# Optimization experiments

Measured on AMD Instinct MI355X. Metric: run time of the kernel, lower is better.

The kernel has to match this reference:

```python
import jax, jax.numpy as jnp
import numpy as np

B, T, D, H = 32, 4096, 512, 512


def setup_inputs() -> dict:
    key = jax.random.key(0)
    ks = jax.random.split(key, 8)
    s = 1.0 / np.sqrt(D)
    return {
        "hidden_state": jax.random.normal(ks[0], (B, D), jnp.float32),
        "encoder_outputs": jax.random.normal(ks[1], (B, T, D), jnp.float32),
        "W": jax.random.normal(ks[2], (D, H), jnp.float32) * s,
        "U": jax.random.normal(ks[3], (D, H), jnp.float32) * s,
        "V": jax.random.normal(ks[4], (H,), jnp.float32) * s,
        "bias": jnp.zeros((H,), jnp.float32),
        "Wa": jax.random.normal(ks[5], (H, H), jnp.float32) * (1.0 / np.sqrt(H)),
        "ba": jnp.zeros((H,), jnp.float32),
    }


def reference(hidden_state, encoder_outputs, W, U, V, bias, Wa, ba):
    # dens1: [B,1,H] ; dens2: [B,T,H]
    dens1 = jnp.einsum('bd,dh->bh', hidden_state, W)[:, None, :]
    dens2 = jnp.einsum('btd,dh->bth', encoder_outputs, U)
    pre = dens1 + dens2 + bias                       # [B,T,H]
    tanh_ = jnp.tanh(jnp.einsum('bth,hk->btk', pre, Wa) + ba)  # extra Dense(tanh)
    cij = jnp.einsum('bth,h->bt', tanh_, V)          # [B,T]
    alphas = jax.nn.softmax(cij, axis=-1)            # [B,T]
    output = jnp.einsum('btd,bt->bd', encoder_outputs, alphas)  # weighted sum
    return output, alphas
```

## Files before the change

### kernel.cpp

```cpp
#include <hip/hip_runtime.h>
#include <hip/hip_bf16.h>


#define BB 32
#define TT 4096
#define DD 512
#define HH 512
#define BK 64

typedef short s16x8 __attribute__((ext_vector_type(8)));
typedef float f32x4 __attribute__((ext_vector_type(4)));

union FU { float f; unsigned u; };

static __device__ __forceinline__ unsigned pack_bf16_trunc(float a, float b) {
    FU ua, ub; ua.f = a; ub.f = b;
    return (ua.u >> 16) | (ub.u & 0xffff0000u);
}

static __device__ __forceinline__ unsigned short f2bf_rne(float x) {
    FU v; v.f = x;
    unsigned u = v.u;
    u = u + 0x7fffu + ((u >> 16) & 1u);
    return (unsigned short)(u >> 16);
}

static __device__ __forceinline__ float tanh_fast(float x) {
    float e = __expf(2.0f * x);
    return 1.0f - 2.0f * __builtin_amdgcn_rcpf(e + 1.0f);
}

static __device__ __forceinline__ void gload_lds16(const void* g, void* l) {
    __builtin_amdgcn_global_load_lds(
        (const __attribute__((address_space(1))) unsigned int*)g,
        (__attribute__((address_space(3))) unsigned int*)l, 16, 0, 0);
}

__global__ void k_dens1(const float* __restrict__ hs, const float* __restrict__ W,
                        const float* __restrict__ bias, float* __restrict__ g) {
    int bi = blockIdx.x;
    int dc = bi & 3, hb = (bi >> 2) & 1, b = bi >> 3;
    int h = hb * 256 + threadIdx.x;
    float s = (dc == 0) ? bias[h] : 0.0f;
    int d0 = dc * 128;
    #pragma unroll 4
    for (int d = 0; d < 128; ++d)
        s = fmaf(hs[b * DD + d0 + d], W[(size_t)(d0 + d) * HH + h], s);
    atomicAdd(&g[b * HH + h], s);
}

__global__ void k_cvec(const float* __restrict__ g, const float* __restrict__ Wa,
                       const float* __restrict__ ba, float* __restrict__ cvec) {
    int bi = blockIdx.x;
    int hc = bi & 3, kb = (bi >> 2) & 1, b = bi >> 3;
    int k = kb * 256 + threadIdx.x;
    float s = (hc == 0) ? ba[k] : 0.0f;
    int h0 = hc * 128;
    #pragma unroll 4
    for (int h = 0; h < 128; ++h)
        s = fmaf(g[b * HH + h0 + h], Wa[(size_t)(h0 + h) * HH + k], s);
    atomicAdd(&cvec[b * HH + k], s);
}

__global__ void k_uwa(const float* __restrict__ U, const float* __restrict__ Wa,
                      unsigned short* __restrict__ UWaT) {
    int d0 = blockIdx.x * 4;
    int tid = threadIdx.x;
    __shared__ float Us[4][DD];
    #pragma unroll
    for (int i = 0; i < 8; ++i) {
        int idx = i * 256 + tid;
        Us[idx >> 9][idx & 511] = U[(size_t)(d0 + (idx >> 9)) * HH + (idx & 511)];
    }
    __syncthreads();
    float acc[4][2] = {};
    #pragma unroll 4
    for (int h = 0; h < DD; ++h) {
        float w0 = Wa[(size_t)h * HH + tid];
        float w1 = Wa[(size_t)h * HH + 256 + tid];
        #pragma unroll
        for (int dd = 0; dd < 4; ++dd) {
            float u = Us[dd][h];
            acc[dd][0] = fmaf(u, w0, acc[dd][0]);
            acc[dd][1] = fmaf(u, w1, acc[dd][1]);
        }
    }
    #pragma unroll
    for (int dd = 0; dd < 4; ++dd) {
        UWaT[(size_t)tid * DD + d0 + dd] = f2bf_rne(acc[dd][0]);
        UWaT[(size_t)(tid + 256) * DD + d0 + dd] = f2bf_rne(acc[dd][1]);
    }
}

__global__ void __launch_bounds__(256, 2) k_gemm_tanh(
    const float* __restrict__ e, const unsigned short* __restrict__ Bt,
    const float* __restrict__ cvec, const float* __restrict__ V,
    float* __restrict__ cij) {
    int tid = threadIdx.x;
    int m0 = blockIdx.x * 64;
    int lane = tid & 63, w = tid >> 6;
    int wn = w * 128;
    int lcol = lane & 15, q = lane >> 4;

    __shared__ __align__(16) unsigned short As[64 * BK];
    __shared__ __align__(16) unsigned short Bs[512 * BK];

    f32x4 acc[4][8] = {};

    const float* Abase = e + (size_t)m0 * DD;

    for (int k0 = 0; k0 < DD; k0 += BK) {
        #pragma unroll
        for (int u = 0; u < 16; ++u) {
            int p = w * 16 + u;
            int g = p >> 3, c0 = (p & 7) * 64;
            const unsigned short* gp = Bt + (size_t)(c0 + lane) * DD + k0 + g * 8;
            gload_lds16(gp, &Bs[(g * 512 + c0) * 8]);
        }
        #pragma unroll
        for (int it = 0; it < 4; ++it) {
            int idx = it * 256 + tid;
            int row = idx >> 4, c4 = idx & 15;
            float4 v = *(const float4*)(Abase + (size_t)row * DD + k0 + c4 * 4);
            uint2 wv;
            wv.x = pack_bf16_trunc(v.x, v.y);
            wv.y = pack_bf16_trunc(v.z, v.w);
            int g = c4 >> 1, half = c4 & 1;
            *(uint2*)&As[(g * 64 + (row ^ g)) * 8 + half * 4] = wv;
        }
        __syncthreads();
        #pragma unroll
        for (int ks = 0; ks < BK; ks += 32) {
            int gk = ks >> 3;
            s16x8 af[4], bfr[8];
            #pragma unroll
            for (int i = 0; i < 4; ++i) {
                int row = i * 16 + lcol, g = gk + q;
                af[i] = *(const s16x8*)&As[(g * 64 + (row ^ g)) * 8];
            }
            #pragma unroll
            for (int j = 0; j < 8; ++j)
                bfr[j] = *(const s16x8*)&Bs[((gk + q) * 512 + wn + j * 16 + lcol) * 8];
            #pragma unroll
            for (int i = 0; i < 4; ++i)
                #pragma unroll
                for (int j = 0; j < 8; ++j)
                    acc[i][j] = __builtin_amdgcn_mfma_f32_16x16x32_bf16(
                        af[i], bfr[j], acc[i][j], 0, 0, 0);
        }
        __syncthreads();
    }

    int b = m0 >> 12;
    float cvv[8], Vv[8];
    #pragma unroll
    for (int j = 0; j < 8; ++j) {
        int h = wn + j * 16 + lcol;
        cvv[j] = cvec[b * HH + h];
        Vv[j] = V[h];
    }
    #pragma unroll
    for (int i = 0; i < 4; ++i) {
        #pragma unroll
        for (int r = 0; r < 4; ++r) {
            float s = 0.0f;
            #pragma unroll
            for (int j = 0; j < 8; ++j)
                s = fmaf(tanh_fast(acc[i][j][r] + cvv[j]), Vv[j], s);
            s += __shfl_xor(s, 1);
            s += __shfl_xor(s, 2);
            s += __shfl_xor(s, 4);
            s += __shfl_xor(s, 8);
            if (lcol == 0)
                atomicAdd(&cij[m0 + i * 16 + q * 4 + r], s);
        }
    }
}

__global__ void k_softmax(const float* __restrict__ cij, float* __restrict__ alphas) {
    int b = blockIdx.x, tid = threadIdx.x;
    const float* row = cij + (size_t)b * TT;
    __shared__ float red[4];
    float m = -1e30f;
    for (int t = tid; t < TT; t += 256) m = fmaxf(m, row[t]);
    #pragma unroll
    for (int o = 1; o < 64; o <<= 1) m = fmaxf(m, __shfl_xor(m, o));
    if ((tid & 63) == 0) red[tid >> 6] = m;
    __syncthreads();
    m = fmaxf(fmaxf(red[0], red[1]), fmaxf(red[2], red[3]));
    __syncthreads();
    float sum = 0.0f;
    for (int t = tid; t < TT; t += 256) sum += __expf(row[t] - m);
    #pragma unroll
    for (int o = 1; o < 64; o <<= 1) sum += __shfl_xor(sum, o);
    if ((tid & 63) == 0) red[tid >> 6] = sum;
    __syncthreads();
    float inv = 1.0f / (red[0] + red[1] + red[2] + red[3]);
    for (int t = tid; t < TT; t += 256)
        alphas[(size_t)b * TT + t] = __expf(row[t] - m) * inv;
}

__global__ void k_wsum(const float* __restrict__ e, const float* __restrict__ alphas,
                       float* __restrict__ out) {
    int b = blockIdx.x >> 6;
    int t0 = (blockIdx.x & 63) * 64;
    int tid = threadIdx.x;
    int half = tid >> 7, f4 = tid & 127;
    const float* base = e + (size_t)b * TT * DD;
    const float* al = alphas + (size_t)b * TT;
    f32x4 a0 = {0, 0, 0, 0}, a1 = {0, 0, 0, 0};
    for (int it = 0; it < 16; ++it) {
        int t = t0 + it * 4 + half;
        float w0 = al[t], w1 = al[t + 2];
        f32x4 v0 = *(const f32x4*)(base + (size_t)t * DD + f4 * 4);
        f32x4 v1 = *(const f32x4*)(base + (size_t)(t + 2) * DD + f4 * 4);
        a0 += w0 * v0;
        a1 += w1 * v1;
    }
    a0 += a1;
    float* o = out + b * DD + f4 * 4;
    atomicAdd(o + 0, a0[0]);
    atomicAdd(o + 1, a0[1]);
    atomicAdd(o + 2, a0[2]);
    atomicAdd(o + 3, a0[3]);
}

extern "C" void kernel_launch(void* const* d_in, const int* in_sizes, int n_in,
                              void* d_out, int out_size, void* d_ws, size_t ws_size,
                              hipStream_t stream) {
    const float* hs   = (const float*)d_in[0];
    const float* e    = (const float*)d_in[1];
    const float* W    = (const float*)d_in[2];
    const float* U    = (const float*)d_in[3];
    const float* V    = (const float*)d_in[4];
    const float* bias = (const float*)d_in[5];
    const float* Wa   = (const float*)d_in[6];
    const float* ba   = (const float*)d_in[7];

    float* out    = (float*)d_out;
    float* alphas = out + BB * DD;

    float*          cij  = (float*)d_ws;
    float*          g    = (float*)((char*)d_ws + 524288);
    float*          cvec = (float*)((char*)d_ws + 589824);
    unsigned short* Bt   = (unsigned short*)((char*)d_ws + 655360);

    hipMemsetAsync(d_ws, 0, 655360, stream);
    hipMemsetAsync(d_out, 0, BB * DD * sizeof(float), stream);

    k_dens1<<<256, 256, 0, stream>>>(hs, W, bias, g);
    k_cvec<<<256, 256, 0, stream>>>(g, Wa, ba, cvec);
    k_uwa<<<128, 256, 0, stream>>>(U, Wa, Bt);
    k_gemm_tanh<<<2048, 256, 0, stream>>>(e, Bt, cvec, V, cij);
    k_softmax<<<BB, 256, 0, stream>>>(cij, alphas);
    k_wsum<<<BB * 64, 256, 0, stream>>>(e, alphas, out);
}
```

Measured before the change: 629.8 us.

## Swizzle B tile layout, prefetch A loads, replace wsum atomics with two-stage reduction

```diff
diff --git a/kernel.cpp b/kernel.cpp
--- a/kernel.cpp
+++ b/kernel.cpp
@@ -64,29 +64,29 @@
 
 __global__ void k_uwa(const float* __restrict__ U, const float* __restrict__ Wa,
                       unsigned short* __restrict__ UWaT) {
-    int d0 = blockIdx.x * 4;
+    int d0 = blockIdx.x * 8;
     int tid = threadIdx.x;
-    __shared__ float Us[4][DD];
-    #pragma unroll
-    for (int i = 0; i < 8; ++i) {
+    __shared__ float Us[8][DD];
+    #pragma unroll
+    for (int i = 0; i < 16; ++i) {
         int idx = i * 256 + tid;
         Us[idx >> 9][idx & 511] = U[(size_t)(d0 + (idx >> 9)) * HH + (idx & 511)];
     }
     __syncthreads();
-    float acc[4][2] = {};
-    #pragma unroll 4
+    float acc[8][2] = {};
+    #pragma unroll 2
     for (int h = 0; h < DD; ++h) {
         float w0 = Wa[(size_t)h * HH + tid];
         float w1 = Wa[(size_t)h * HH + 256 + tid];
         #pragma unroll
-        for (int dd = 0; dd < 4; ++dd) {
+        for (int dd = 0; dd < 8; ++dd) {
             float u = Us[dd][h];
             acc[dd][0] = fmaf(u, w0, acc[dd][0]);
             acc[dd][1] = fmaf(u, w1, acc[dd][1]);
         }
     }
     #pragma unroll
-    for (int dd = 0; dd < 4; ++dd) {
+    for (int dd = 0; dd < 8; ++dd) {
         UWaT[(size_t)tid * DD + d0 + dd] = f2bf_rne(acc[dd][0]);
         UWaT[(size_t)(tid + 256) * DD + d0 + dd] = f2bf_rne(acc[dd][1]);
     }
@@ -101,6 +101,7 @@
     int lane = tid & 63, w = tid >> 6;
     int wn = w * 128;
     int lcol = lane & 15, q = lane >> 4;
+    int rl = lane >> 3, gg = lane & 7;
 
     __shared__ __align__(16) unsigned short As[64 * BK];
     __shared__ __align__(16) unsigned short Bs[512 * BK];
@@ -110,21 +111,27 @@
     const float* Abase = e + (size_t)m0 * DD;
 
     for (int k0 = 0; k0 < DD; k0 += BK) {
-        #pragma unroll
-        for (int u = 0; u < 16; ++u) {
-            int p = w * 16 + u;
-            int g = p >> 3, c0 = (p & 7) * 64;
-            const unsigned short* gp = Bt + (size_t)(c0 + lane) * DD + k0 + g * 8;
-            gload_lds16(gp, &Bs[(g * 512 + c0) * 8]);
-        }
+        float4 av[4];
         #pragma unroll
         for (int it = 0; it < 4; ++it) {
             int idx = it * 256 + tid;
             int row = idx >> 4, c4 = idx & 15;
-            float4 v = *(const float4*)(Abase + (size_t)row * DD + k0 + c4 * 4);
+            av[it] = *(const float4*)(Abase + (size_t)row * DD + k0 + c4 * 4);
+        }
+        #pragma unroll
+        for (int u = 0; u < 16; ++u) {
+            int n0 = w * 128 + u * 8;
+            const unsigned short* gp =
+                Bt + (size_t)(n0 + rl) * DD + k0 + ((gg ^ rl) << 3);
+            gload_lds16(gp, &Bs[n0 * 64]);
+        }
+        #pragma unroll
+        for (int it = 0; it < 4; ++it) {
+            int idx = it * 256 + tid;
+            int row = idx >> 4, c4 = idx & 15;
             uint2 wv;
-            wv.x = pack_bf16_trunc(v.x, v.y);
-            wv.y = pack_bf16_trunc(v.z, v.w);
+            wv.x = pack_bf16_trunc(av[it].x, av[it].y);
+            wv.y = pack_bf16_trunc(av[it].z, av[it].w);
             int g = c4 >> 1, half = c4 & 1;
             *(uint2*)&As[(g * 64 + (row ^ g)) * 8 + half * 4] = wv;
         }
@@ -139,8 +146,10 @@
                 af[i] = *(const s16x8*)&As[(g * 64 + (row ^ g)) * 8];
             }
             #pragma unroll
-            for (int j = 0; j < 8; ++j)
-                bfr[j] = *(const s16x8*)&Bs[((gk + q) * 512 + wn + j * 16 + lcol) * 8];
+            for (int j = 0; j < 8; ++j) {
+                int col = wn + j * 16 + lcol, g = gk + q;
+                bfr[j] = *(const s16x8*)&Bs[col * 64 + ((g ^ (col & 7)) << 3)];
+            }
             #pragma unroll
             for (int i = 0; i < 4; ++i)
                 #pragma unroll
@@ -201,9 +210,10 @@
 }
 
 __global__ void k_wsum(const float* __restrict__ e, const float* __restrict__ alphas,
-                       float* __restrict__ out) {
+                       float* __restrict__ pw) {
     int b = blockIdx.x >> 6;
-    int t0 = (blockIdx.x & 63) * 64;
+    int chunk = blockIdx.x & 63;
+    int t0 = chunk * 64;
     int tid = threadIdx.x;
     int half = tid >> 7, f4 = tid & 127;
     const float* base = e + (size_t)b * TT * DD;
@@ -218,11 +228,26 @@
         a1 += w1 * v1;
     }
     a0 += a1;
-    float* o = out + b * DD + f4 * 4;
-    atomicAdd(o + 0, a0[0]);
-    atomicAdd(o + 1, a0[1]);
-    atomicAdd(o + 2, a0[2]);
-    atomicAdd(o + 3, a0[3]);
+    __shared__ f32x4 red[128];
+    if (half == 1) red[f4] = a0;
+    __syncthreads();
+    if (half == 0) {
+        a0 += red[f4];
+        *(f32x4*)&pw[((size_t)(b * 64 + chunk)) * DD + f4 * 4] = a0;
+    }
+}
+
+__global__ void k_wred(const float* __restrict__ pw, float* __restrict__ out) {
+    int b = blockIdx.x, tid = threadIdx.x;
+    float2 acc = {0.0f, 0.0f};
+    const float* base = pw + (size_t)b * 64 * DD;
+    #pragma unroll 4
+    for (int c = 0; c < 64; ++c) {
+        float2 v = *(const float2*)(base + (size_t)c * DD + tid * 2);
+        acc.x += v.x;
+        acc.y += v.y;
+    }
+    *(float2*)&out[b * DD + tid * 2] = acc;
 }
 
 extern "C" void kernel_launch(void* const* d_in, const int* in_sizes, int n_in,
@@ -244,14 +269,15 @@
     float*          g    = (float*)((char*)d_ws + 524288);
     float*          cvec = (float*)((char*)d_ws + 589824);
     unsigned short* Bt   = (unsigned short*)((char*)d_ws + 655360);
+    float*          pw   = (float*)((char*)d_ws + 1179648);
 
     hipMemsetAsync(d_ws, 0, 655360, stream);
-    hipMemsetAsync(d_out, 0, BB * DD * sizeof(float), stream);
 
     k_dens1<<<256, 256, 0, stream>>>(hs, W, bias, g);
     k_cvec<<<256, 256, 0, stream>>>(g, Wa, ba, cvec);
-    k_uwa<<<128, 256, 0, stream>>>(U, Wa, Bt);
+    k_uwa<<<64, 256, 0, stream>>>(U, Wa, Bt);
     k_gemm_tanh<<<2048, 256, 0, stream>>>(e, Bt, cvec, V, cij);
     k_softmax<<<BB, 256, 0, stream>>>(cij, alphas);
-    k_wsum<<<BB * 64, 256, 0, stream>>>(e, alphas, out);
-}
+    k_wsum<<<BB * 64, 256, 0, stream>>>(e, alphas, pw);
+    k_wred<<<BB, 256, 0, stream>>>(pw, out);
+}
```

Measured after the change: 567.7 us. 1.11x faster.
